# Kernel tuning notes

Measured on AMD Instinct MI355X. Metric: run time of the kernel, lower is better.

The kernel has to match this reference:

```python
import jax, jax.numpy as jnp
import numpy as np

N_NODES = 100000
N_EDGES = 3200000
N_ELEMS = 10


def setup_inputs() -> dict:
    key = jax.random.key(0)
    k1, k2, k3, k4, k5 = jax.random.split(key, 5)
    # edge distances in (0.1, 5.1) Angstrom, shape [E, 1]
    x = jax.random.uniform(k1, (N_EDGES, 1), dtype=jnp.float32) * 5.0 + 0.1
    # one-hot-ish node element encoding; only argmax matters
    node_attrs = jax.random.normal(k2, (N_NODES, N_ELEMS), dtype=jnp.float32)
    edge_index = jax.random.randint(k3, (2, N_EDGES), 0, N_NODES)
    # atomic numbers of the chemical species present (1..89)
    atomic_numbers = jax.random.randint(k4, (N_ELEMS,), 1, 90)
    # stand-in for ase.data.covalent_radii (119 entries, ~0.3..2.3 A)
    covalent_radii = jax.random.uniform(k5, (119,), dtype=jnp.float32) * 2.0 + 0.3
    return {
        "x": x,
        "node_attrs": node_attrs,
        "edge_index": edge_index,
        "atomic_numbers": atomic_numbers,
        "covalent_radii": covalent_radii,
    }


def _polynomial_envelope(x, r_max, p):
    # PolynomialCutoff.calculate_envelope, p = 6
    r = x / r_max
    env = (1.0
           - (p + 1.0) * (p + 2.0) / 2.0 * jnp.power(r, p)
           + p * (p + 2.0) * jnp.power(r, p + 1)
           - p * (p + 1.0) / 2.0 * jnp.power(r, p + 2))
    return env * (x < r_max)


def reference(x, node_attrs, edge_index, atomic_numbers, covalent_radii):
    c = jnp.array([0.1818, 0.5099, 0.2802, 0.02817], dtype=jnp.float32)
    p = 6.0
    a_exp = jnp.float32(0.3)
    a_prefactor = jnp.float32(0.4543)

    sender, receiver = edge_index[0], edge_index[1]
    # per-node atomic number from one-hot attrs, [N, 1]
    node_Z = atomic_numbers[jnp.argmax(node_attrs, axis=1)][..., None]
    Z_u = node_Z[sender].astype(jnp.int32)  # [E, 1]
    Z_v = node_Z[receiver].astype(jnp.int32)  # [E, 1]
    Zu_f = Z_u.astype(jnp.float32)
    Zv_f = Z_v.astype(jnp.float32)

    a = a_prefactor * 0.529 / (jnp.power(Zu_f, a_exp) + jnp.power(Zv_f, a_exp))
    r_over_a = x / a  # [E, 1]
    phi = (c[0] * jnp.exp(-3.2 * r_over_a)
           + c[1] * jnp.exp(-0.9423 * r_over_a)
           + c[2] * jnp.exp(-0.4028 * r_over_a)
           + c[3] * jnp.exp(-0.2016 * r_over_a))
    v_edges = 14.3996 * Zu_f * Zv_f / x * phi  # [E, 1]

    r_max = covalent_radii[Z_u] + covalent_radii[Z_v]  # [E, 1]
    envelope = _polynomial_envelope(x, r_max, p)
    v_edges = 0.5 * v_edges * envelope  # [E, 1]

    # scatter-sum edge energies into receiver nodes -> [N]
    V_ZBL = jax.ops.segment_sum(v_edges[:, 0], receiver,
                                num_segments=node_attrs.shape[0])
    return V_ZBL
```

## Files before the change

kernel.cpp:

```cpp
#include <hip/hip_runtime.h>
#include <stdint.h>

#define N_NODES 100000
#define N_ELEM_PAD 100096
#define N_EDGES 3200000
#define N_ELEMS 10
#define N_PAIRS (N_ELEMS * N_ELEMS)

#define NB 256
#define NPB 391
#define SCAT_THREADS 1024
#define EPT 4
#define EPB (SCAT_THREADS * EPT)
#define NBLK ((N_EDGES + EPB - 1) / EPB)
#define NG4 (N_EDGES / 4)
#define PREP_BLOCKS 391

#define L_REC   0
#define L_ELEM  16384
#define L_TAB   (16384 + 100096)
#define L_CNT   (L_TAB + 1600)
#define L_OFF   (L_CNT + 1024)
#define LDS_BYTES (L_OFF + 1024)

__global__ __launch_bounds__(256) void prep_kernel(
    const float* __restrict__ node_attrs,
    const int* __restrict__ atomic_numbers,
    const float* __restrict__ covalent_radii,
    uint8_t* __restrict__ node_elem,
    float4* __restrict__ pair_tab) {
  int i = blockIdx.x * 256 + threadIdx.x;

  if (blockIdx.x == 0 && threadIdx.x < N_PAIRS) {
    int t = threadIdx.x;
    int eu = t / N_ELEMS, ev = t % N_ELEMS;
    float Zuf = (float)atomic_numbers[eu];
    float Zvf = (float)atomic_numbers[ev];
    float a = 0.4543f * 0.529f / (powf(Zuf, 0.3f) + powf(Zvf, 0.3f));
    float rmax = covalent_radii[(int)Zuf] + covalent_radii[(int)Zvf];
    pair_tab[t] = make_float4(1.0f / a, 0.5f * 14.3996f * Zuf * Zvf,
                              rmax, 1.0f / rmax);
  }

  if (i < N_NODES) {
    const float2* row = (const float2*)(node_attrs + (size_t)i * N_ELEMS);
    float best = -INFINITY;
    int bj = 0;
#pragma unroll
    for (int k = 0; k < 5; ++k) {
      float2 v = row[k];
      if (v.x > best) { best = v.x; bj = 2 * k; }
      if (v.y > best) { best = v.y; bj = 2 * k + 1; }
    }
    node_elem[i] = (uint8_t)bj;
  }
}

__device__ __forceinline__ float edge_val(float xi, int u, int v,
                                          const uint8_t* s_elem,
                                          const float4* s_tab) {
  int eu = s_elem[u];
  int ev = s_elem[v];
  float4 tb = s_tab[eu * N_ELEMS + ev];
  float roa = xi * tb.x;
  float phi = 0.1818f  * __expf(-3.2f    * roa)
            + 0.5099f  * __expf(-0.9423f * roa)
            + 0.2802f  * __expf(-0.4028f * roa)
            + 0.02817f * __expf(-0.2016f * roa);
  float val = tb.y * phi / xi;
  float r  = xi * tb.w;
  float r2 = r * r;
  float r6 = r2 * r2 * r2;
  float env = 1.0f - 28.0f * r6 + 48.0f * r6 * r - 21.0f * r6 * r2;
  return (xi < tb.z) ? val * env : 0.0f;
}

__global__ __launch_bounds__(SCAT_THREADS) void scatter_kernel(
    const float* __restrict__ x,
    const int* __restrict__ edge_index,
    const uint8_t* __restrict__ node_elem,
    const float4* __restrict__ pair_tab,
    unsigned int* __restrict__ dir,
    unsigned int* __restrict__ records) {
  extern __shared__ char smem[];
  unsigned int* s_rec  = (unsigned int*)(smem + L_REC);
  uint8_t*      s_elem = (uint8_t*)(smem + L_ELEM);
  float4*       s_tab  = (float4*)(smem + L_TAB);
  unsigned int* s_cnt  = (unsigned int*)(smem + L_CNT);
  unsigned int* s_off  = (unsigned int*)(smem + L_OFF);

  int tid = threadIdx.x;

  int g4 = blockIdx.x * SCAT_THREADS + tid;
  bool ok = g4 < NG4;
  int e = g4 * 4;
  float4 xv = make_float4(1, 1, 1, 1);
  int4 uu = make_int4(0, 0, 0, 0), vv = make_int4(0, 0, 0, 0);
  if (ok) {
    xv = *(const float4*)(x + e);
    uu = *(const int4*)(edge_index + e);
    vv = *(const int4*)(edge_index + N_EDGES + e);
  }

  {
    const uint4* src = (const uint4*)node_elem;
    uint4* dst = (uint4*)s_elem;
#pragma unroll
    for (int j = tid; j < N_ELEM_PAD / 16; j += SCAT_THREADS) dst[j] = src[j];
  }
  if (tid < N_PAIRS) s_tab[tid] = pair_tab[tid];
  if (tid < NB) s_cnt[tid] = 0u;
  __syncthreads();

  float val[EPT];
  unsigned int pk[EPT];
  {
    int rv[4] = {vv.x, vv.y, vv.z, vv.w};
    int ru[4] = {uu.x, uu.y, uu.z, uu.w};
    float xs[4] = {xv.x, xv.y, xv.z, xv.w};
#pragma unroll
    for (int c = 0; c < 4; ++c) {
      if (ok) {
        val[c] = edge_val(xs[c], ru[c], rv[c], s_elem, s_tab);
        unsigned int b = (unsigned int)rv[c] / NPB;
        unsigned int lid = (unsigned int)rv[c] - b * NPB;
        pk[c] = (b << 21) | lid;
      } else {
        pk[c] = 0xFFFFFFFFu;
      }
    }
  }

#pragma unroll
  for (int c = 0; c < EPT; ++c) {
    if (pk[c] != 0xFFFFFFFFu) {
      unsigned int b = pk[c] >> 21;
      unsigned int r = atomicAdd(&s_cnt[b], 1u);
      pk[c] |= (r << 9);
    }
  }
  __syncthreads();

  if (tid < 64) {
    unsigned int c0 = s_cnt[tid * 4 + 0];
    unsigned int c1 = s_cnt[tid * 4 + 1];
    unsigned int c2 = s_cnt[tid * 4 + 2];
    unsigned int c3 = s_cnt[tid * 4 + 3];
    unsigned int local = c0 + c1 + c2 + c3;
    unsigned int inc = local;
#pragma unroll
    for (int d = 1; d < 64; d <<= 1) {
      unsigned int t = __shfl_up((int)inc, d, 64);
      if (tid >= d) inc += t;
    }
    unsigned int excl = inc - local;
    s_off[tid * 4 + 0] = excl;
    s_off[tid * 4 + 1] = excl + c0;
    s_off[tid * 4 + 2] = excl + c0 + c1;
    s_off[tid * 4 + 3] = excl + c0 + c1 + c2;
  }
  __syncthreads();

  if (tid < NB)
    dir[(size_t)blockIdx.x * NB + tid] = (s_off[tid] << 13) | s_cnt[tid];

#pragma unroll
  for (int c = 0; c < EPT; ++c) {
    if (pk[c] != 0xFFFFFFFFu) {
      unsigned int b = pk[c] >> 21;
      unsigned int r = (pk[c] >> 9) & 0xFFFu;
      unsigned int lid = pk[c] & 0x1FFu;
      s_rec[s_off[b] + r] = (__float_as_uint(val[c]) & ~0x1FFu) | lid;
    }
  }
  __syncthreads();

  {
    uint4* dst = (uint4*)(records + (size_t)blockIdx.x * EPB);
    const uint4* src = (const uint4*)s_rec;
    dst[tid] = src[tid];
  }
}

__global__ __launch_bounds__(1024) void reduce_kernel(
    const unsigned int* __restrict__ dir,
    const unsigned int* __restrict__ records,
    float* __restrict__ out) {
  __shared__ float bins[NPB];
  int b = blockIdx.x, tid = threadIdx.x;

  if (tid < NPB) bins[tid] = 0.0f;
  __syncthreads();

  if (tid < NBLK) {
    unsigned int d = dir[(size_t)tid * NB + b];
    unsigned int c = d & 0x1FFFu;
    unsigned int o = d >> 13;
    const unsigned int* seg = records + (size_t)tid * EPB + o;
    for (unsigned int i = 0; i < c; ++i) {
      unsigned int rec = seg[i];
      atomicAdd(&bins[rec & 0x1FFu], __uint_as_float(rec & ~0x1FFu));
    }
  }
  __syncthreads();

  int nb0 = b * NPB;
  if (tid < NPB && nb0 + tid < N_NODES) out[nb0 + tid] = bins[tid];
}

extern "C" void kernel_launch(void* const* d_in, const int* in_sizes, int n_in,
                              void* d_out, int out_size, void* d_ws, size_t ws_size,
                              hipStream_t stream) {
  const float* x              = (const float*)d_in[0];
  const float* node_attrs     = (const float*)d_in[1];
  const int*   edge_index     = (const int*)d_in[2];
  const int*   atomic_numbers = (const int*)d_in[3];
  const float* covalent_radii = (const float*)d_in[4];
  float* out = (float*)d_out;

  char* wsp = (char*)d_ws;
  unsigned int* records   = (unsigned int*)wsp;
  unsigned int* dir       = (unsigned int*)(wsp + 12812288);
  float4*       pair_tab  = (float4*)(wsp + 13613056);
  uint8_t*      node_elem = (uint8_t*)(wsp + 13614656);

  prep_kernel<<<PREP_BLOCKS, 256, 0, stream>>>(
      node_attrs, atomic_numbers, covalent_radii, node_elem, pair_tab);

  scatter_kernel<<<NBLK, SCAT_THREADS, LDS_BYTES, stream>>>(
      x, edge_index, node_elem, pair_tab, dir, records);

  reduce_kernel<<<NB, 1024, 0, stream>>>(dir, records, out);
}
```

Baseline: 125.3 us.

## Enlarge scatter tiles to one block per CU and split reduce segments across threads

The scatter kernel now runs 256 blocks of 12,500 edges each (16 edges per thread) instead of 782 blocks of 4,096. That cuts the repeated copy of the 100 KB per-node element table into LDS by about three times, and the whole launch fits in a single wave of blocks. The record bit-packing widens the rank and offset fields to cover the larger per-block bucket counts. In the reduce kernel, four threads now share each segment, so every 1024-thread block uses all its threads on the 256 segments. The trade-offs are LDS use close to the per-CU limit and fewer resident waves to hide memory latency.

```diff
diff --git a/kernel.cpp b/kernel.cpp
--- a/kernel.cpp
+++ b/kernel.cpp
@@ -10,15 +10,14 @@
 #define NB 256
 #define NPB 391
 #define SCAT_THREADS 1024
-#define EPT 4
-#define EPB (SCAT_THREADS * EPT)
-#define NBLK ((N_EDGES + EPB - 1) / EPB)
-#define NG4 (N_EDGES / 4)
+#define EPB 12500
+#define NBLK 256
+#define NGROUPS (EPB / 4)
 #define PREP_BLOCKS 391
 
 #define L_REC   0
-#define L_ELEM  16384
-#define L_TAB   (16384 + 100096)
+#define L_ELEM  50000
+#define L_TAB   (50000 + 100096)
 #define L_CNT   (L_TAB + 1600)
 #define L_OFF   (L_CNT + 1024)
 #define LDS_BYTES (L_OFF + 1024)
@@ -91,52 +90,45 @@
 
   int tid = threadIdx.x;
 
-  int g4 = blockIdx.x * SCAT_THREADS + tid;
-  bool ok = g4 < NG4;
-  int e = g4 * 4;
-  float4 xv = make_float4(1, 1, 1, 1);
-  int4 uu = make_int4(0, 0, 0, 0), vv = make_int4(0, 0, 0, 0);
-  if (ok) {
-    xv = *(const float4*)(x + e);
-    uu = *(const int4*)(edge_index + e);
-    vv = *(const int4*)(edge_index + N_EDGES + e);
-  }
-
   {
     const uint4* src = (const uint4*)node_elem;
     uint4* dst = (uint4*)s_elem;
-#pragma unroll
     for (int j = tid; j < N_ELEM_PAD / 16; j += SCAT_THREADS) dst[j] = src[j];
   }
   if (tid < N_PAIRS) s_tab[tid] = pair_tab[tid];
   if (tid < NB) s_cnt[tid] = 0u;
   __syncthreads();
 
-  float val[EPT];
-  unsigned int pk[EPT];
-  {
+  float val[16];
+  unsigned int pk[16];
+
+#pragma unroll
+  for (int k = 0; k < 4; ++k) {
+    int gl = k * SCAT_THREADS + tid;
+    bool ok = gl < NGROUPS;
+    int e = (blockIdx.x * NGROUPS + gl) * 4;
+    float4 xv = make_float4(1, 1, 1, 1);
+    int4 uu = make_int4(0, 0, 0, 0), vv = make_int4(0, 0, 0, 0);
+    if (ok) {
+      xv = *(const float4*)(x + e);
+      uu = *(const int4*)(edge_index + e);
+      vv = *(const int4*)(edge_index + N_EDGES + e);
+    }
     int rv[4] = {vv.x, vv.y, vv.z, vv.w};
     int ru[4] = {uu.x, uu.y, uu.z, uu.w};
     float xs[4] = {xv.x, xv.y, xv.z, xv.w};
 #pragma unroll
     for (int c = 0; c < 4; ++c) {
+      int j = k * 4 + c;
       if (ok) {
-        val[c] = edge_val(xs[c], ru[c], rv[c], s_elem, s_tab);
+        val[j] = edge_val(xs[c], ru[c], rv[c], s_elem, s_tab);
         unsigned int b = (unsigned int)rv[c] / NPB;
         unsigned int lid = (unsigned int)rv[c] - b * NPB;
-        pk[c] = (b << 21) | lid;
+        unsigned int r = atomicAdd(&s_cnt[b], 1u);
+        pk[j] = (b << 23) | (r << 9) | lid;
       } else {
-        pk[c] = 0xFFFFFFFFu;
+        pk[j] = 0xFFFFFFFFu;
       }
-    }
-  }
-
-#pragma unroll
-  for (int c = 0; c < EPT; ++c) {
-    if (pk[c] != 0xFFFFFFFFu) {
-      unsigned int b = pk[c] >> 21;
-      unsigned int r = atomicAdd(&s_cnt[b], 1u);
-      pk[c] |= (r << 9);
     }
   }
   __syncthreads();
@@ -162,15 +154,15 @@
   __syncthreads();
 
   if (tid < NB)
-    dir[(size_t)blockIdx.x * NB + tid] = (s_off[tid] << 13) | s_cnt[tid];
-
-#pragma unroll
-  for (int c = 0; c < EPT; ++c) {
-    if (pk[c] != 0xFFFFFFFFu) {
-      unsigned int b = pk[c] >> 21;
-      unsigned int r = (pk[c] >> 9) & 0xFFFu;
-      unsigned int lid = pk[c] & 0x1FFu;
-      s_rec[s_off[b] + r] = (__float_as_uint(val[c]) & ~0x1FFu) | lid;
+    dir[(size_t)blockIdx.x * NB + tid] = (s_off[tid] << 14) | s_cnt[tid];
+
+#pragma unroll
+  for (int j = 0; j < 16; ++j) {
+    if (pk[j] != 0xFFFFFFFFu) {
+      unsigned int b = pk[j] >> 23;
+      unsigned int r = (pk[j] >> 9) & 0x3FFFu;
+      unsigned int lid = pk[j] & 0x1FFu;
+      s_rec[s_off[b] + r] = (__float_as_uint(val[j]) & ~0x1FFu) | lid;
     }
   }
   __syncthreads();
@@ -178,7 +170,7 @@
   {
     uint4* dst = (uint4*)(records + (size_t)blockIdx.x * EPB);
     const uint4* src = (const uint4*)s_rec;
-    dst[tid] = src[tid];
+    for (int j = tid; j < EPB / 4; j += SCAT_THREADS) dst[j] = src[j];
   }
 }
 
@@ -192,15 +184,15 @@
   if (tid < NPB) bins[tid] = 0.0f;
   __syncthreads();
 
-  if (tid < NBLK) {
-    unsigned int d = dir[(size_t)tid * NB + b];
-    unsigned int c = d & 0x1FFFu;
-    unsigned int o = d >> 13;
-    const unsigned int* seg = records + (size_t)tid * EPB + o;
-    for (unsigned int i = 0; i < c; ++i) {
-      unsigned int rec = seg[i];
-      atomicAdd(&bins[rec & 0x1FFu], __uint_as_float(rec & ~0x1FFu));
-    }
+  int seg = tid >> 2;
+  int sub = tid & 3;
+  unsigned int d = dir[(size_t)seg * NB + b];
+  unsigned int c = d & 0x3FFFu;
+  unsigned int o = d >> 14;
+  const unsigned int* sp = records + (size_t)seg * EPB + o;
+  for (unsigned int i = sub; i < c; i += 4) {
+    unsigned int rec = sp[i];
+    atomicAdd(&bins[rec & 0x1FFu], __uint_as_float(rec & ~0x1FFu));
   }
   __syncthreads();
 
@@ -220,9 +212,9 @@
 
   char* wsp = (char*)d_ws;
   unsigned int* records   = (unsigned int*)wsp;
-  unsigned int* dir       = (unsigned int*)(wsp + 12812288);
-  float4*       pair_tab  = (float4*)(wsp + 13613056);
-  uint8_t*      node_elem = (uint8_t*)(wsp + 13614656);
+  unsigned int* dir       = (unsigned int*)(wsp + 12800000);
+  float4*       pair_tab  = (float4*)(wsp + 13062144);
+  uint8_t*      node_elem = (uint8_t*)(wsp + 13063744);
 
   prep_kernel<<<PREP_BLOCKS, 256, 0, stream>>>(
       node_attrs, atomic_numbers, covalent_radii, node_elem, pair_tab);
```

New measurement: 118.8 us. -5.2%, faster.
